# Kernel optimization log

Measured on AMD Instinct MI355X. Metric: run time of the kernel, lower is better.

Reference implementation:

```python
import jax, jax.numpy as jnp
import numpy as np

B, S, D0, D, H = 8, 1024, 128, 256, 8
HD = D // H  # head_dim = 32


def setup_inputs() -> dict:
    key = jax.random.key(0)
    k0, k1, k2, k3, k4, k5 = jax.random.split(key, 6)
    query = jax.random.normal(k0, (B, S, D0), dtype=jnp.float32)
    U = jax.random.normal(k1, (B, H, S, S), dtype=jnp.float32)
    # nn.Linear(in, out, bias=False) weights have shape (out, in)
    sc = 1.0 / np.sqrt(D0)
    Wq = jax.random.normal(k2, (D, D0), dtype=jnp.float32) * sc
    Wk = jax.random.normal(k3, (D, D0), dtype=jnp.float32) * sc
    Wv = jax.random.normal(k4, (D, D0), dtype=jnp.float32) * sc
    Wo = jax.random.normal(k5, (D0, D), dtype=jnp.float32) * (1.0 / np.sqrt(D))
    return {"query": query, "U": U, "Wq": Wq, "Wk": Wk, "Wv": Wv, "Wo": Wo}


def reference(query, U, Wq, Wk, Wv, Wo):
    b, s, _ = query.shape
    # projections: y = x @ W.T ; split heads -> (B, H, S, HD)
    def proj(W):
        y = jnp.einsum('bsd,ed->bse', query, W)
        return y.reshape(b, s, H, HD).transpose(0, 2, 1, 3)

    Q, K, V = proj(Wq), proj(Wk), proj(Wv)
    scale = jnp.sqrt(jnp.asarray(HD, dtype=jnp.float32))
    scores = (jnp.einsum('bhqd,bhkd->bhqk', Q, K) + U) / scale  # (B,H,S,S)
    # mask computed from Q (as in original): key positions where Q rows sum to 0
    mask = (Q.sum(axis=-1) != 0)[:, :, None, :]  # (B,H,1,S), broadcasts over queries
    scores = jnp.where(mask, scores, -jnp.inf)
    attn = jax.nn.softmax(scores, axis=-1)
    out = jnp.einsum('bhqk,bhkd->bhqd', attn, V)  # (B,H,S,HD)
    out = out.transpose(0, 2, 1, 3).reshape(b, s, H * HD)
    output = jnp.einsum('bse,oe->bso', out, Wo)  # (B,S,D0)
    return output, attn
```

## Files before the change

### kernel.cpp

```cpp
#include <hip/hip_runtime.h>
#include <stdint.h>
#include <math.h>

#define B_ 8
#define S_ 1024
#define D0_ 128
#define D_ 256
#define H_ 8
#define HD_ 32
#define BH_ (B_*H_)

typedef __attribute__((ext_vector_type(8))) short short8;
typedef __attribute__((ext_vector_type(4))) float f32x4;
typedef __attribute__((ext_vector_type(4))) unsigned int u32x4;
typedef __attribute__((ext_vector_type(2))) float f32x2;

__device__ __forceinline__ unsigned short f2bf(float x) {
    unsigned int u = __float_as_uint(x);
    u += 0x7FFFu + ((u >> 16) & 1u);
    return (unsigned short)(u >> 16);
}
__device__ __forceinline__ float bf2f(unsigned short s) {
    return __uint_as_float(((unsigned int)s) << 16);
}

__global__ __launch_bounds__(256) void proj_kernel(
    const float* __restrict__ query,
    const float* __restrict__ Wq, const float* __restrict__ Wk, const float* __restrict__ Wv,
    unsigned short* __restrict__ Qhi, unsigned short* __restrict__ Qlo,
    unsigned short* __restrict__ Khi, unsigned short* __restrict__ Klo,
    unsigned short* __restrict__ Vt)
{
    const int z = blockIdx.z;
    const float* W = (z == 0) ? Wq : (z == 1) ? Wk : Wv;
    const int m0 = blockIdx.x * 64;
    const int n0 = blockIdx.y * 64;
    __shared__ float xs[64 * 68];
    __shared__ float ws[64 * 68];
    const int t = threadIdx.x;
    const int ty = t >> 4, tx = t & 15;
    float acc[4][4] = {};
    for (int kc = 0; kc < 128; kc += 64) {
        #pragma unroll
        for (int it = 0; it < 4; ++it) {
            int fi = t + it * 256;
            int row = fi >> 4, c4 = fi & 15;
            *(float4*)(&xs[row * 68 + c4 * 4]) = *(const float4*)(&query[(size_t)(m0 + row) * 128 + kc + c4 * 4]);
            *(float4*)(&ws[row * 68 + c4 * 4]) = *(const float4*)(&W[(size_t)(n0 + row) * 128 + kc + c4 * 4]);
        }
        __syncthreads();
        #pragma unroll
        for (int k4 = 0; k4 < 16; ++k4) {
            float4 a4[4], b4[4];
            #pragma unroll
            for (int i = 0; i < 4; ++i) a4[i] = *(const float4*)(&xs[(ty * 4 + i) * 68 + k4 * 4]);
            #pragma unroll
            for (int j = 0; j < 4; ++j) b4[j] = *(const float4*)(&ws[(tx * 4 + j) * 68 + k4 * 4]);
            #pragma unroll
            for (int i = 0; i < 4; ++i)
                #pragma unroll
                for (int j = 0; j < 4; ++j)
                    acc[i][j] += a4[i].x * b4[j].x + a4[i].y * b4[j].y + a4[i].z * b4[j].z + a4[i].w * b4[j].w;
        }
        __syncthreads();
    }
    #pragma unroll
    for (int i = 0; i < 4; ++i) {
        int m = m0 + ty * 4 + i;
        int b = m >> 10, s = m & 1023;
        #pragma unroll
        for (int j = 0; j < 4; ++j) {
            int o = n0 + tx * 4 + j;
            int h = o >> 5, d = o & 31;
            int bh = b * 8 + h;
            float y = acc[i][j];
            if (z < 2) {
                unsigned short hi = f2bf(y);
                unsigned short lo = f2bf(y - bf2f(hi));
                size_t idx = ((size_t)(bh * 1024 + s)) * 32 + d;
                if (z == 0) { Qhi[idx] = hi; Qlo[idx] = lo; }
                else        { Khi[idx] = hi; Klo[idx] = lo; }
            } else {
                Vt[((size_t)(bh * 32 + d)) * 1024 + s] = f2bf(y);
            }
        }
    }
}

__global__ void mask_kernel(const unsigned short* __restrict__ Qhi,
                            const unsigned short* __restrict__ Qlo,
                            float* __restrict__ maskbias)
{
    int r = blockIdx.x * blockDim.x + threadIdx.x;
    if (r >= BH_ * S_) return;
    const unsigned short* ph = Qhi + (size_t)r * 32;
    const unsigned short* pl = Qlo + (size_t)r * 32;
    float s = 0.f;
    #pragma unroll
    for (int d = 0; d < 32; ++d) s += bf2f(ph[d]) + bf2f(pl[d]);
    maskbias[r] = (s != 0.0f) ? 0.0f : -INFINITY;
}

__global__ __launch_bounds__(256, 3) void attn_kernel(
    const unsigned short* __restrict__ Qhi, const unsigned short* __restrict__ Qlo,
    const unsigned short* __restrict__ Khi, const unsigned short* __restrict__ Klo,
    const unsigned short* __restrict__ Vt, const float* __restrict__ maskbias,
    const float* __restrict__ U, float* __restrict__ attn_out, float* __restrict__ out_buf)
{
    __shared__ float Ored[4 * 16 * 36];
    __shared__ float redMS[4][2][16];

    const int bid = blockIdx.x;
    const int swz = (bid & 7) * 512 + (bid >> 3);
    const int bh = swz >> 6;
    const int qbase = (swz & 63) << 4;
    const int tid = threadIdx.x;
    const int wid = tid >> 6;
    const int c = tid & 15;
    const int g = (tid >> 4) & 3;
    const int kstrip = wid << 8;

    const size_t bh_qk = (size_t)bh * S_ * 32;
    const size_t bh_u = (size_t)bh * S_ * S_;
    const int q = qbase + c;

    const float* Urow = U + bh_u + (size_t)q * S_;
    f32x4 u[16];
    #pragma unroll
    for (int kf = 0; kf < 16; ++kf)
        u[kf] = *(const f32x4*)(Urow + kstrip + kf * 16 + g * 4);

    short8 qh = *(const short8*)(Qhi + bh_qk + (size_t)q * 32 + 8 * g);
    short8 ql = *(const short8*)(Qlo + bh_qk + (size_t)q * 32 + 8 * g);

    f32x4 s[16];
    #pragma unroll
    for (int kf = 0; kf < 16; ++kf) s[kf] = (f32x4){0.f, 0.f, 0.f, 0.f};

    #pragma unroll
    for (int kf = 0; kf < 16; ++kf) {
        size_t koff = bh_qk + (size_t)(kstrip + kf * 16 + c) * 32 + 8 * g;
        short8 kh = *(const short8*)(Khi + koff);
        short8 kl = *(const short8*)(Klo + koff);
        s[kf] = __builtin_amdgcn_mfma_f32_16x16x32_bf16(kh, qh, s[kf], 0, 0, 0);
        s[kf] = __builtin_amdgcn_mfma_f32_16x16x32_bf16(kl, qh, s[kf], 0, 0, 0);
        s[kf] = __builtin_amdgcn_mfma_f32_16x16x32_bf16(kh, ql, s[kf], 0, 0, 0);
    }

    const float inv_scale = 0.17677669529663687f;
    const float* mbrow = maskbias + bh * S_;
    #pragma unroll
    for (int kf = 0; kf < 16; ++kf) {
        int k0 = kstrip + kf * 16 + g * 4;
        f32x4 mb = *(const f32x4*)(mbrow + k0);
        #pragma unroll
        for (int r = 0; r < 4; ++r)
            s[kf][r] = (s[kf][r] + u[kf][r]) * inv_scale + mb[r];
    }

    float m = s[0][0];
    #pragma unroll
    for (int kf = 0; kf < 16; ++kf)
        #pragma unroll
        for (int r = 0; r < 4; ++r) m = fmaxf(m, s[kf][r]);
    m = fmaxf(m, __shfl_xor(m, 16, 64));
    m = fmaxf(m, __shfl_xor(m, 32, 64));
    m = fmaxf(m, -1e30f);

    float sum = 0.f;
    #pragma unroll
    for (int kf = 0; kf < 16; ++kf)
        #pragma unroll
        for (int r = 0; r < 4; ++r) {
            float p = __expf(s[kf][r] - m);
            s[kf][r] = p;
            sum += p;
        }
    sum += __shfl_xor(sum, 16, 64);
    sum += __shfl_xor(sum, 32, 64);
    if (g == 0) { redMS[wid][0][c] = m; redMS[wid][1][c] = sum; }
    __syncthreads();

    float m0 = redMS[0][0][c], m1 = redMS[1][0][c], m2 = redMS[2][0][c], m3 = redMS[3][0][c];
    float M = fmaxf(fmaxf(m0, m1), fmaxf(m2, m3));
    float S = redMS[0][1][c] * __expf(m0 - M) + redMS[1][1][c] * __expf(m1 - M)
            + redMS[2][1][c] * __expf(m2 - M) + redMS[3][1][c] * __expf(m3 - M);
    const float fw = __expf(m - M) / S;

    const int srcA = c + 32 * (g & 1);
    const int srcB = srcA + 16;
    const int gd2 = g >> 1;
    f32x4 o0 = (f32x4){0.f, 0.f, 0.f, 0.f};
    f32x4 o1 = (f32x4){0.f, 0.f, 0.f, 0.f};
    const unsigned short* vb0 = Vt + (size_t)(bh * 32 + c) * 1024 + kstrip;
    const unsigned short* vb1 = vb0 + 16 * 1024;
    #pragma unroll
    for (int ch = 0; ch < 8; ++ch) {
        unsigned int p0[2], p1[2];
        p0[0] = __builtin_amdgcn_perm(__float_as_uint(s[2 * ch][1]), __float_as_uint(s[2 * ch][0]), 0x07060302u);
        p0[1] = __builtin_amdgcn_perm(__float_as_uint(s[2 * ch][3]), __float_as_uint(s[2 * ch][2]), 0x07060302u);
        p1[0] = __builtin_amdgcn_perm(__float_as_uint(s[2 * ch + 1][1]), __float_as_uint(s[2 * ch + 1][0]), 0x07060302u);
        p1[1] = __builtin_amdgcn_perm(__float_as_uint(s[2 * ch + 1][3]), __float_as_uint(s[2 * ch + 1][2]), 0x07060302u);
        unsigned int b0A = (unsigned int)__shfl((int)p0[0], srcA, 64);
        unsigned int b1A = (unsigned int)__shfl((int)p0[1], srcA, 64);
        unsigned int b0B = (unsigned int)__shfl((int)p0[0], srcB, 64);
        unsigned int b1B = (unsigned int)__shfl((int)p0[1], srcB, 64);
        unsigned int c0A = (unsigned int)__shfl((int)p1[0], srcA, 64);
        unsigned int c1A = (unsigned int)__shfl((int)p1[1], srcA, 64);
        unsigned int c0B = (unsigned int)__shfl((int)p1[0], srcB, 64);
        unsigned int c1B = (unsigned int)__shfl((int)p1[1], srcB, 64);
        union { u32x4 u; short8 h; } bb;
        bb.u[0] = gd2 ? c0A : b0A;
        bb.u[1] = gd2 ? c1A : b1A;
        bb.u[2] = gd2 ? c0B : b0B;
        bb.u[3] = gd2 ? c1B : b1B;
        short8 A0 = *(const short8*)(vb0 + ch * 32 + g * 8);
        short8 A1 = *(const short8*)(vb1 + ch * 32 + g * 8);
        o0 = __builtin_amdgcn_mfma_f32_16x16x32_bf16(A0, bb.h, o0, 0, 0, 0);
        o1 = __builtin_amdgcn_mfma_f32_16x16x32_bf16(A1, bb.h, o1, 0, 0, 0);
    }
    #pragma unroll
    for (int r = 0; r < 4; ++r) { o0[r] *= fw; o1[r] *= fw; }
    *(f32x4*)(&Ored[(wid * 16 + c) * 36 + g * 4]) = o0;
    *(f32x4*)(&Ored[(wid * 16 + c) * 36 + 16 + g * 4]) = o1;
    __syncthreads();

    const int qq = tid >> 4;
    const int dd = (tid & 15) * 2;
    float v0 = 0.f, v1 = 0.f;
    #pragma unroll
    for (int w = 0; w < 4; ++w) {
        v0 += Ored[(w * 16 + qq) * 36 + dd];
        v1 += Ored[(w * 16 + qq) * 36 + dd + 1];
    }
    const int b = bh >> 3, h = bh & 7;
    f32x2 vv = {v0, v1};
    *(f32x2*)(out_buf + ((size_t)(b * 1024 + qbase + qq)) * 256 + h * 32 + dd) = vv;

    float* arow = attn_out + bh_u + (size_t)q * S_;
    #pragma unroll
    for (int kf = 0; kf < 16; ++kf) {
        int k0 = kstrip + kf * 16 + g * 4;
        f32x4 a;
        #pragma unroll
        for (int r = 0; r < 4; ++r) a[r] = s[kf][r] * fw;
        *(f32x4*)(arow + k0) = a;
    }
}

__global__ __launch_bounds__(256) void outproj_kernel(
    const float* __restrict__ xb, const float* __restrict__ Wo, float* __restrict__ outp)
{
    const int m0 = blockIdx.x * 64;
    const int n0 = blockIdx.y * 64;
    __shared__ float xs[64 * 68];
    __shared__ float ws[64 * 68];
    const int t = threadIdx.x;
    const int ty = t >> 4, tx = t & 15;
    float acc[4][4] = {};
    for (int kc = 0; kc < 256; kc += 64) {
        #pragma unroll
        for (int it = 0; it < 4; ++it) {
            int fi = t + it * 256;
            int row = fi >> 4, c4 = fi & 15;
            *(float4*)(&xs[row * 68 + c4 * 4]) = *(const float4*)(&xb[(size_t)(m0 + row) * 256 + kc + c4 * 4]);
            *(float4*)(&ws[row * 68 + c4 * 4]) = *(const float4*)(&Wo[(size_t)(n0 + row) * 256 + kc + c4 * 4]);
        }
        __syncthreads();
        #pragma unroll
        for (int k4 = 0; k4 < 16; ++k4) {
            float4 a4[4], b4[4];
            #pragma unroll
            for (int i = 0; i < 4; ++i) a4[i] = *(const float4*)(&xs[(ty * 4 + i) * 68 + k4 * 4]);
            #pragma unroll
            for (int j = 0; j < 4; ++j) b4[j] = *(const float4*)(&ws[(tx * 4 + j) * 68 + k4 * 4]);
            #pragma unroll
            for (int i = 0; i < 4; ++i)
                #pragma unroll
                for (int j = 0; j < 4; ++j)
                    acc[i][j] += a4[i].x * b4[j].x + a4[i].y * b4[j].y + a4[i].z * b4[j].z + a4[i].w * b4[j].w;
        }
        __syncthreads();
    }
    #pragma unroll
    for (int i = 0; i < 4; ++i)
        #pragma unroll
        for (int j = 0; j < 4; ++j)
            outp[(size_t)(m0 + ty * 4 + i) * 128 + n0 + tx * 4 + j] = acc[i][j];
}

extern "C" void kernel_launch(void* const* d_in, const int* in_sizes, int n_in,
                              void* d_out, int out_size, void* d_ws, size_t ws_size,
                              hipStream_t stream)
{
    const float* query = (const float*)d_in[0];
    const float* U     = (const float*)d_in[1];
    const float* Wq    = (const float*)d_in[2];
    const float* Wk    = (const float*)d_in[3];
    const float* Wv    = (const float*)d_in[4];
    const float* Wo    = (const float*)d_in[5];

    float* output = (float*)d_out;
    float* attn   = (float*)d_out + (size_t)B_ * S_ * D0_;

    const size_t NQK = (size_t)BH_ * S_ * 32;
    unsigned short* Qhi = (unsigned short*)d_ws;
    unsigned short* Qlo = Qhi + NQK;
    unsigned short* Khi = Qlo + NQK;
    unsigned short* Klo = Khi + NQK;
    unsigned short* Vt  = Klo + NQK;
    float* maskbias = (float*)(Vt + NQK);
    float* out_buf  = maskbias + (size_t)BH_ * S_;

    proj_kernel<<<dim3(128, 4, 3), 256, 0, stream>>>(query, Wq, Wk, Wv, Qhi, Qlo, Khi, Klo, Vt);
    mask_kernel<<<dim3(256), 256, 0, stream>>>(Qhi, Qlo, maskbias);
    attn_kernel<<<dim3(4096), 256, 0, stream>>>(Qhi, Qlo, Khi, Klo, Vt, maskbias, U, attn, out_buf);
    outproj_kernel<<<dim3(128, 2), 256, 0, stream>>>(out_buf, Wo, output);
}
```

Before: 261.7 us.

## Fuse mask computation into projection and seed MFMA accumulators with U

```diff
diff --git a/kernel.cpp b/kernel.cpp
--- a/kernel.cpp
+++ b/kernel.cpp
@@ -29,7 +29,7 @@
     const float* __restrict__ Wq, const float* __restrict__ Wk, const float* __restrict__ Wv,
     unsigned short* __restrict__ Qhi, unsigned short* __restrict__ Qlo,
     unsigned short* __restrict__ Khi, unsigned short* __restrict__ Klo,
-    unsigned short* __restrict__ Vt)
+    unsigned short* __restrict__ Vt, float* __restrict__ maskbias)
 {
     const int z = blockIdx.z;
     const float* W = (z == 0) ? Wq : (z == 1) ? Wk : Wv;
@@ -37,8 +37,10 @@
     const int n0 = blockIdx.y * 64;
     __shared__ float xs[64 * 68];
     __shared__ float ws[64 * 68];
+    __shared__ float msum[64][2];
     const int t = threadIdx.x;
     const int ty = t >> 4, tx = t & 15;
+    if (z == 0 && t < 128) msum[t >> 1][t & 1] = 0.f;
     float acc[4][4] = {};
     for (int kc = 0; kc < 128; kc += 64) {
         #pragma unroll
@@ -85,23 +87,24 @@
             }
         }
     }
-}
-
-__global__ void mask_kernel(const unsigned short* __restrict__ Qhi,
-                            const unsigned short* __restrict__ Qlo,
-                            float* __restrict__ maskbias)
-{
-    int r = blockIdx.x * blockDim.x + threadIdx.x;
-    if (r >= BH_ * S_) return;
-    const unsigned short* ph = Qhi + (size_t)r * 32;
-    const unsigned short* pl = Qlo + (size_t)r * 32;
-    float s = 0.f;
-    #pragma unroll
-    for (int d = 0; d < 32; ++d) s += bf2f(ph[d]) + bf2f(pl[d]);
-    maskbias[r] = (s != 0.0f) ? 0.0f : -INFINITY;
-}
-
-__global__ __launch_bounds__(256, 3) void attn_kernel(
+    if (z == 0) {
+        #pragma unroll
+        for (int i = 0; i < 4; ++i) {
+            float ps = acc[i][0] + acc[i][1] + acc[i][2] + acc[i][3];
+            atomicAdd(&msum[ty * 4 + i][tx >> 3], ps);
+        }
+        __syncthreads();
+        if (t < 128) {
+            int row = t >> 1, hh = t & 1;
+            int m = m0 + row;
+            int b = m >> 10, s = m & 1023;
+            int bh = b * 8 + (n0 >> 5) + hh;
+            maskbias[bh * 1024 + s] = (msum[row][hh] != 0.0f) ? 0.0f : -INFINITY;
+        }
+    }
+}
+
+__global__ __launch_bounds__(256, 4) void attn_kernel(
     const unsigned short* __restrict__ Qhi, const unsigned short* __restrict__ Qlo,
     const unsigned short* __restrict__ Khi, const unsigned short* __restrict__ Klo,
     const unsigned short* __restrict__ Vt, const float* __restrict__ maskbias,
@@ -125,17 +128,13 @@
     const int q = qbase + c;
 
     const float* Urow = U + bh_u + (size_t)q * S_;
-    f32x4 u[16];
+    f32x4 s[16];
     #pragma unroll
     for (int kf = 0; kf < 16; ++kf)
-        u[kf] = *(const f32x4*)(Urow + kstrip + kf * 16 + g * 4);
+        s[kf] = *(const f32x4*)(Urow + kstrip + kf * 16 + g * 4);
 
     short8 qh = *(const short8*)(Qhi + bh_qk + (size_t)q * 32 + 8 * g);
     short8 ql = *(const short8*)(Qlo + bh_qk + (size_t)q * 32 + 8 * g);
-
-    f32x4 s[16];
-    #pragma unroll
-    for (int kf = 0; kf < 16; ++kf) s[kf] = (f32x4){0.f, 0.f, 0.f, 0.f};
 
     #pragma unroll
     for (int kf = 0; kf < 16; ++kf) {
@@ -155,7 +154,7 @@
         f32x4 mb = *(const f32x4*)(mbrow + k0);
         #pragma unroll
         for (int r = 0; r < 4; ++r)
-            s[kf][r] = (s[kf][r] + u[kf][r]) * inv_scale + mb[r];
+            s[kf][r] = s[kf][r] * inv_scale + mb[r];
     }
 
     float m = s[0][0];
@@ -312,8 +311,7 @@
     float* maskbias = (float*)(Vt + NQK);
     float* out_buf  = maskbias + (size_t)BH_ * S_;
 
-    proj_kernel<<<dim3(128, 4, 3), 256, 0, stream>>>(query, Wq, Wk, Wv, Qhi, Qlo, Khi, Klo, Vt);
-    mask_kernel<<<dim3(256), 256, 0, stream>>>(Qhi, Qlo, maskbias);
+    proj_kernel<<<dim3(128, 4, 3), 256, 0, stream>>>(query, Wq, Wk, Wv, Qhi, Qlo, Khi, Klo, Vt, maskbias);
     attn_kernel<<<dim3(4096), 256, 0, stream>>>(Qhi, Qlo, Khi, Klo, Vt, maskbias, U, attn, out_buf);
     outproj_kernel<<<dim3(128, 2), 256, 0, stream>>>(out_buf, Wo, output);
 }
```

Measured after the change: 259.4 us. About the same (-0.9%).
